# Kernel optimization log

Hardware: AMD Instinct MI355X
Metric: run time of the kernel (lower is better)

Reference implementation:

```python
import jax, jax.numpy as jnp
import numpy as np

THRESHOLD = 0.5
NEG_POS_RATIO = 3
ALPHA = 1.0
N_CLASSES = 81


def xy_to_cxcy(xy):
    return jnp.concatenate([(xy[..., :2] + xy[..., 2:]) / 2.0,
                            xy[..., 2:] - xy[..., :2]], axis=-1)


def cxcy_to_xy(cxcy):
    return jnp.concatenate([cxcy[..., :2] - cxcy[..., 2:] / 2.0,
                            cxcy[..., :2] + cxcy[..., 2:] / 2.0], axis=-1)


def cxcy_to_gcxgcy(cxcy, priors_cxcy):
    # SSD encoding with standard variances (0.1 for center, 0.2 for size)
    g_cxcy = (cxcy[..., :2] - priors_cxcy[..., :2]) / (priors_cxcy[..., 2:] / 10.0)
    g_wh = jnp.log(cxcy[..., 2:] / priors_cxcy[..., 2:]) * 5.0
    return jnp.concatenate([g_cxcy, g_wh], axis=-1)


def iou_pairwise(a_xy, b_xy):
    # a_xy: (N, O, 4), b_xy: (P, 4) -> (N, O, P)
    lt = jnp.maximum(a_xy[..., :, None, :2], b_xy[None, None, :, :2])
    rb = jnp.minimum(a_xy[..., :, None, 2:], b_xy[None, None, :, 2:])
    wh = jnp.clip(rb - lt, 0.0)
    inter = wh[..., 0] * wh[..., 1]
    area_a = (a_xy[..., 2] - a_xy[..., 0]) * (a_xy[..., 3] - a_xy[..., 1])
    area_b = (b_xy[:, 2] - b_xy[:, 0]) * (b_xy[:, 3] - b_xy[:, 1])
    union = area_a[..., :, None] + area_b[None, None, :] - inter
    return inter / union


def setup_inputs() -> dict:
    key = jax.random.key(0)
    k1, k2, k3, k4, k5, k6, k7 = jax.random.split(key, 7)
    N, P, C, O = 32, 8732, N_CLASSES, 16
    predicted_locs = jax.random.normal(k1, (N, P, 4), dtype=jnp.float32)
    predicted_scores = jax.random.normal(k2, (N, P, C), dtype=jnp.float32)
    # ground-truth boxes: build valid cxcy then convert to xy in [0, 1]
    b_cxy = jax.random.uniform(k3, (N, O, 2), minval=0.2, maxval=0.8)
    b_wh = jax.random.uniform(k4, (N, O, 2), minval=0.05, maxval=0.3)
    boxes = cxcy_to_xy(jnp.concatenate([b_cxy, b_wh], axis=-1)).astype(jnp.float32)
    labels = jax.random.randint(k5, (N, O), 1, C).astype(jnp.int32)  # 0 = background
    # priors in cxcy, valid (positive wh)
    p_cxy = jax.random.uniform(k6, (P, 2), minval=0.05, maxval=0.95)
    p_wh = jax.random.uniform(k7, (P, 2), minval=0.05, maxval=0.4)
    priors_cxcy = jnp.concatenate([p_cxy, p_wh], axis=-1).astype(jnp.float32)
    return {"predicted_locs": predicted_locs, "predicted_scores": predicted_scores,
            "boxes": boxes, "labels": labels, "priors_cxcy": priors_cxcy}


def reference(predicted_locs, predicted_scores, boxes, labels, priors_cxcy):
    N, P, C = predicted_scores.shape
    O = boxes.shape[1]
    priors_xy = cxcy_to_xy(priors_cxcy)  # (P, 4)

    overlap = iou_pairwise(boxes, priors_xy)            # (N, O, P)
    overlap_for_each_prior = overlap.max(axis=1)        # (N, P)
    object_for_each_prior = overlap.argmax(axis=1)      # (N, P)
    prior_for_each_object = overlap.argmax(axis=2)      # (N, O)

    obj_ids = jnp.arange(O)

    def assign(ofp, ovl, pfo):
        # force each object to be matched to its best prior with overlap 1
        ofp = ofp.at[pfo].set(obj_ids)
        ovl = ovl.at[pfo].set(1.0)
        return ofp, ovl

    object_for_each_prior, overlap_for_each_prior = jax.vmap(assign)(
        object_for_each_prior, overlap_for_each_prior, prior_for_each_object)

    label_for_each_prior = jnp.take_along_axis(labels, object_for_each_prior, axis=1)  # (N, P)
    true_classes = jnp.where(overlap_for_each_prior < THRESHOLD, 0, label_for_each_prior)

    matched_boxes = jnp.take_along_axis(
        boxes, object_for_each_prior[..., None], axis=1)  # (N, P, 4)
    true_locs = cxcy_to_gcxgcy(xy_to_cxcy(matched_boxes), priors_cxcy)

    positive = true_classes != 0                          # (N, P)
    pos_f = positive.astype(predicted_locs.dtype)

    # localization loss (L1, reduction='none' in original despite the name)
    loc_per_prior = jnp.abs(predicted_locs - true_locs).sum(axis=-1)  # (N, P)
    n_pos_total = pos_f.sum()
    loc_loss = (loc_per_prior * pos_f).sum() / (4.0 * n_pos_total)

    # confidence loss (cross entropy per prior)
    logp = jax.nn.log_softmax(predicted_scores, axis=-1)
    ce = -jnp.take_along_axis(logp, true_classes[..., None], axis=-1)[..., 0]  # (N, P)

    conf_loss_pos = (ce * pos_f).sum()
    ce_neg = jnp.where(positive, 0.0, ce)
    ce_neg_sorted = -jnp.sort(-ce_neg, axis=1)            # descending
    n_positives = positive.sum(axis=1)                    # (N,)
    hard = (jnp.arange(P)[None, :] < (NEG_POS_RATIO * n_positives)[:, None]).astype(ce.dtype)
    conf_loss_hard_neg = (ce_neg_sorted * hard).sum()
    conf_loss = (conf_loss_hard_neg + conf_loss_pos) / n_pos_total

    return conf_loss + ALPHA * loc_loss
```

## Files before the change

kernel.cpp:

```cpp
#include <hip/hip_runtime.h>
#include <hip/hip_bf16.h>
#include <stdint.h>

#define BLOCK 256
#define MAXO 64
#define TK_THREADS 1024
#define CK_MAX 4096

__global__ void match_object_kernel(const float* __restrict__ boxes,
                                    const float* __restrict__ priors,
                                    int* __restrict__ pfop,
                                    float* __restrict__ acc, int* __restrict__ n_pos,
                                    unsigned* __restrict__ done, int N, int P, int O) {
    __shared__ unsigned long long swm[4];
    int idx = blockIdx.x, tid = threadIdx.x;
    if (idx == 0) {
        for (int j = tid; j < N; j += BLOCK) n_pos[j] = 0;
        if (tid >= 64 && tid < 67) acc[tid - 64] = 0.f;
        if (tid == 96) *done = 0u;
    }
    const float* b = boxes + (size_t)idx * 4;
    float bx0 = b[0], by0 = b[1], bx1 = b[2], by1 = b[3];
    float areaa = (bx1 - bx0) * (by1 - by0);

    unsigned long long best = 0ULL;
    for (int p = tid; p < P; p += BLOCK) {
        float4 pr = ((const float4*)priors)[p];
        float px0 = pr.x - pr.z * 0.5f, py0 = pr.y - pr.w * 0.5f;
        float px1 = pr.x + pr.z * 0.5f, py1 = pr.y + pr.w * 0.5f;
        float areab = (px1 - px0) * (py1 - py0);
        float ltx = fmaxf(bx0, px0), lty = fmaxf(by0, py0);
        float rbx = fminf(bx1, px1), rby = fminf(by1, py1);
        float wx = fmaxf(rbx - ltx, 0.f), wy = fmaxf(rby - lty, 0.f);
        float inter = wx * wy;
        float iou = inter / (areaa + areab - inter);
        unsigned long long cand = (((unsigned long long)__float_as_uint(iou)) << 32) |
                                  (unsigned long long)(0xFFFFFFFFu - (unsigned)p);
        if (cand > best) best = cand;
    }
    #pragma unroll
    for (int off = 32; off >= 1; off >>= 1) {
        unsigned long long other = __shfl_down(best, off);
        if (other > best) best = other;
    }
    if ((tid & 63) == 0) swm[tid >> 6] = best;
    __syncthreads();
    if (tid == 0) {
        unsigned long long r = swm[0];
        for (int w = 1; w < BLOCK / 64; ++w) if (swm[w] > r) r = swm[w];
        pfop[idx] = (int)(0xFFFFFFFFu - (unsigned)(r & 0xFFFFFFFFull));
    }
}

__global__ void __launch_bounds__(256, 4)
fused_match_ce_kernel(const float* __restrict__ boxes,
                      const float* __restrict__ priors,
                      const float* __restrict__ locs,
                      const int* __restrict__ labels,
                      const int* __restrict__ pfop,
                      const float* __restrict__ scores,
                      float* __restrict__ ce_neg,
                      float* __restrict__ acc, int* __restrict__ n_pos,
                      int N, int P, int O) {
    __shared__ float sbx[MAXO * 4];
    __shared__ float sarea[MAXO];
    __shared__ int   spf[MAXO];
    __shared__ int   slab[MAXO];
    __shared__ float sredf[8];
    __shared__ int   sredi[4];
    int n = blockIdx.y, tid = threadIdx.x;
    if (tid < O * 4) sbx[tid] = boxes[(size_t)n * O * 4 + tid];
    if (tid >= 128 && tid < 128 + O) spf[tid - 128]  = pfop[n * O + (tid - 128)];
    if (tid >= 192 && tid < 192 + O) slab[tid - 192] = labels[n * O + (tid - 192)];
    __syncthreads();
    if (tid < O)
        sarea[tid] = (sbx[tid*4+2] - sbx[tid*4+0]) * (sbx[tid*4+3] - sbx[tid*4+1]);
    __syncthreads();

    int p = blockIdx.x * BLOCK + tid;
    bool valid = p < P;
    float my_loc = 0.f, my_pce = 0.f; int my_pos = 0;

    if (valid) {
        size_t t = (size_t)n * P + p;

        float4 pr = ((const float4*)priors)[p];

        int lane = tid & 63;
        int s = lane & 3;
        const float4* q = (const float4*)scores + (t >> 2) * 81;
        int g0q = (s == 0) ? 0 : (20 * s + 1);
        const float4* qa = q + g0q;

        float4 v[19];
        #pragma unroll
        for (int j = 0; j < 19; ++j) v[j] = qa[j];
        float4 v19 = q[19];
        float4 vb  = q[20 * (s + 1)];
        __builtin_amdgcn_sched_barrier(0);

        float px0 = pr.x - pr.z * 0.5f, py0 = pr.y - pr.w * 0.5f;
        float px1 = pr.x + pr.z * 0.5f, py1 = pr.y + pr.w * 0.5f;
        float areab = (px1 - px0) * (py1 - py0);

        float best = -1.f; int bo = 0;
        for (int o = 0; o < O; ++o) {
            float ltx = fmaxf(sbx[o*4+0], px0);
            float lty = fmaxf(sbx[o*4+1], py0);
            float rbx = fminf(sbx[o*4+2], px1);
            float rby = fminf(sbx[o*4+3], py1);
            float wx = fmaxf(rbx - ltx, 0.f), wy = fmaxf(rby - lty, 0.f);
            float inter = wx * wy;
            float iou = inter / (sarea[o] + areab - inter);
            if (iou > best) { best = iou; bo = o; }
        }
        int fo = -1;
        for (int o = 0; o < O; ++o) if (spf[o] == p) fo = o;
        int obj; float ov;
        if (fo >= 0) { obj = fo; ov = 1.0f; }
        else         { obj = bo; ov = best; }
        int tc = (ov < 0.5f) ? 0 : slab[obj];
        if (tc != 0) {
            my_pos = 1;
            float x0 = sbx[obj*4+0], y0 = sbx[obj*4+1], x1 = sbx[obj*4+2], y1 = sbx[obj*4+3];
            float cx = (x0 + x1) * 0.5f, cy = (y0 + y1) * 0.5f;
            float w = x1 - x0, h = y1 - y0;
            float g0 = (cx - pr.x) / (pr.z / 10.0f);
            float g1 = (cy - pr.y) / (pr.w / 10.0f);
            float g2 = logf(w / pr.z) * 5.0f;
            float g3 = logf(h / pr.w) * 5.0f;
            const float* pl = locs + t * 4;
            my_loc = fabsf(pl[0]-g0) + fabsf(pl[1]-g1) + fabsf(pl[2]-g2) + fabsf(pl[3]-g3);
        }

        float a0 = 0.f, a1 = 0.f, a2 = 0.f, a3 = 0.f;
        #pragma unroll
        for (int j = 0; j < 19; ++j) {
            a0 += __expf(v[j].x); a1 += __expf(v[j].y);
            a2 += __expf(v[j].z); a3 += __expf(v[j].w);
        }
        float A = (a0 + a1) + (a2 + a3);
        if (s == 0) A += __expf(v19.x) + __expf(v19.y) + __expf(v19.z) + __expf(v19.w);
        float B = 0.f;
        {
            float ex = __expf(vb.x), ey = __expf(vb.y), ez = __expf(vb.z), ew = __expf(vb.w);
            A += ex;
            A += (s >= 1) ? ey : 0.f;   B += (s >= 1) ? 0.f : ey;
            A += (s >= 2) ? ez : 0.f;   B += (s >= 2) ? 0.f : ez;
            A += (s == 3) ? ew : 0.f;   B += (s == 3) ? 0.f : ew;
        }
        int src = (lane & ~3) | ((s + 3) & 3);
        float l = A + __shfl(B, src);

        float stc = scores[t * 81 + tc];
        float ce = logf(l) - stc;
        ce_neg[t] = (tc != 0) ? 0.f : ce;
        if (tc != 0) my_pce = ce;
    }

    #pragma unroll
    for (int off = 32; off >= 1; off >>= 1) {
        my_loc += __shfl_down(my_loc, off);
        my_pce += __shfl_down(my_pce, off);
        my_pos += __shfl_down(my_pos, off);
    }
    if ((tid & 63) == 0) {
        int w = tid >> 6;
        sredf[w] = my_loc; sredf[4 + w] = my_pce; sredi[w] = my_pos;
    }
    __syncthreads();
    if (tid == 0) {
        float L  = (sredf[0] + sredf[1]) + (sredf[2] + sredf[3]);
        float Pp = (sredf[4] + sredf[5]) + (sredf[6] + sredf[7]);
        int  np  = sredi[0] + sredi[1] + sredi[2] + sredi[3];
        if (L  != 0.f) atomicAdd(&acc[0], L);
        if (Pp != 0.f) atomicAdd(&acc[1], Pp);
        if (np)        atomicAdd(&n_pos[n], np);
    }
}

__global__ void match_prior_kernel(const float* __restrict__ boxes,
                                   const float* __restrict__ priors,
                                   const float* __restrict__ locs,
                                   const int* __restrict__ labels,
                                   const int* __restrict__ pfop,
                                   int* __restrict__ tcarr,
                                   float* __restrict__ acc, int* __restrict__ n_pos,
                                   int N, int P, int O) {
    __shared__ float sbx[MAXO * 4];
    __shared__ float sarea[MAXO];
    __shared__ int   spf[MAXO];
    __shared__ int   slab[MAXO];
    int n = blockIdx.y, tid = threadIdx.x;
    if (tid < O * 4) sbx[tid] = boxes[(size_t)n * O * 4 + tid];
    if (tid >= 128 && tid < 128 + O) spf[tid - 128]  = pfop[n * O + (tid - 128)];
    if (tid >= 192 && tid < 192 + O) slab[tid - 192] = labels[n * O + (tid - 192)];
    __syncthreads();
    if (tid < O)
        sarea[tid] = (sbx[tid*4+2] - sbx[tid*4+0]) * (sbx[tid*4+3] - sbx[tid*4+1]);
    __syncthreads();

    int p = blockIdx.x * BLOCK + tid;
    bool valid = p < P;
    float my_loc = 0.f; int my_pos = 0;
    if (valid) {
        float4 pr = ((const float4*)priors)[p];
        float px0 = pr.x - pr.z * 0.5f, py0 = pr.y - pr.w * 0.5f;
        float px1 = pr.x + pr.z * 0.5f, py1 = pr.y + pr.w * 0.5f;
        float areab = (px1 - px0) * (py1 - py0);

        float best = -1.f; int bo = 0;
        for (int o = 0; o < O; ++o) {
            float ltx = fmaxf(sbx[o*4+0], px0);
            float lty = fmaxf(sbx[o*4+1], py0);
            float rbx = fminf(sbx[o*4+2], px1);
            float rby = fminf(sbx[o*4+3], py1);
            float wx = fmaxf(rbx - ltx, 0.f), wy = fmaxf(rby - lty, 0.f);
            float inter = wx * wy;
            float iou = inter / (sarea[o] + areab - inter);
            if (iou > best) { best = iou; bo = o; }
        }
        int fo = -1;
        for (int o = 0; o < O; ++o) if (spf[o] == p) fo = o;
        int obj; float ov;
        if (fo >= 0) { obj = fo; ov = 1.0f; }
        else         { obj = bo; ov = best; }
        int lab = slab[obj];
        int tc = (ov < 0.5f) ? 0 : lab;
        tcarr[(size_t)n * P + p] = tc;
        if (tc != 0) {
            my_pos = 1;
            float x0 = sbx[obj*4+0], y0 = sbx[obj*4+1], x1 = sbx[obj*4+2], y1 = sbx[obj*4+3];
            float cx = (x0 + x1) * 0.5f, cy = (y0 + y1) * 0.5f;
            float w = x1 - x0, h = y1 - y0;
            float g0 = (cx - pr.x) / (pr.z / 10.0f);
            float g1 = (cy - pr.y) / (pr.w / 10.0f);
            float g2 = logf(w / pr.z) * 5.0f;
            float g3 = logf(h / pr.w) * 5.0f;
            const float* pl = locs + ((size_t)n * P + p) * 4;
            my_loc = fabsf(pl[0]-g0) + fabsf(pl[1]-g1) + fabsf(pl[2]-g2) + fabsf(pl[3]-g3);
        }
    }
    #pragma unroll
    for (int off = 32; off >= 1; off >>= 1) {
        my_loc += __shfl_down(my_loc, off);
        my_pos += __shfl_down(my_pos, off);
    }
    if ((tid & 63) == 0 && my_pos) {
        atomicAdd(&acc[0], my_loc);
        atomicAdd(&n_pos[n], my_pos);
    }
}

__global__ void loss_generic_kernel(const float* __restrict__ scores,
                                    const int* __restrict__ tcarr,
                                    float* __restrict__ ce_neg, float* __restrict__ acc,
                                    int NP, int C) {
    int t = blockIdx.x * blockDim.x + threadIdx.x;
    if (t >= NP) return;
    int tc = tcarr[t];
    const float* s = scores + (size_t)t * C;
    float m = -3.0e38f;
    for (int j = 0; j < C; ++j) m = fmaxf(m, s[j]);
    float l = 0.f, stc = 0.f;
    for (int j = 0; j < C; ++j) {
        float v = s[j];
        l += __expf(v - m);
        if (j == tc) stc = v;
    }
    float ce = m + logf(l) - stc;
    bool pos = (tc != 0);
    ce_neg[t] = pos ? 0.f : ce;
    if (pos) atomicAdd(&acc[1], ce);
}

__global__ void topk_final_kernel(const float* __restrict__ ce_neg,
                                  const int* __restrict__ n_pos,
                                  float* __restrict__ acc, unsigned* __restrict__ done,
                                  int N, int P, unsigned* __restrict__ out) {
    __shared__ unsigned skeys[8732];
    __shared__ int hist[4096];
    __shared__ int part[1024];
    __shared__ int s_tb, s_ca, s_tb2, s_ca2, s_cnt;
    __shared__ float shf[16];
    int n = blockIdx.x, tid = threadIdx.x;
    int k = 3 * n_pos[n]; if (k > P) k = P;
    float bsum = 0.f;

    if (k > 0) {
        const float* row = ce_neg + (size_t)n * P;
        for (int i = tid; i < P; i += TK_THREADS) skeys[i] = __float_as_uint(row[i]);
        #pragma unroll
        for (int b = 0; b < 4; ++b) hist[tid * 4 + b] = 0;
        __syncthreads();

        for (int i = tid; i < P; i += TK_THREADS) atomicAdd(&hist[skeys[i] >> 20], 1);
        __syncthreads();
        int h0 = hist[tid*4], h1 = hist[tid*4+1], h2 = hist[tid*4+2], h3 = hist[tid*4+3];
        part[tid] = h0 + h1 + h2 + h3;
        __syncthreads();
        for (int s = 1; s < 1024; s <<= 1) {
            int v = part[tid] + ((tid + s < 1024) ? part[tid + s] : 0);
            __syncthreads();
            part[tid] = v;
            __syncthreads();
        }
        int sfx = (tid + 1 < 1024) ? part[tid + 1] : 0;
        int sf3 = sfx, sf2 = sfx + h3, sf1 = sf2 + h2, sf0 = sf1 + h1;
        if (sf0 < k && k <= sf0 + h0) { s_tb = tid*4;   s_ca = sf0; }
        if (sf1 < k && k <= sf1 + h1) { s_tb = tid*4+1; s_ca = sf1; }
        if (sf2 < k && k <= sf2 + h2) { s_tb = tid*4+2; s_ca = sf2; }
        if (sf3 < k && k <= sf3 + h3) { s_tb = tid*4+3; s_ca = sf3; }
        __syncthreads();
        int tb = s_tb, kk = k - s_ca;

        if (tid < 256) part[tid] = 0;
        __syncthreads();
        float ssum = 0.f;
        for (int i = tid; i < P; i += TK_THREADS) {
            unsigned key = skeys[i];
            int bin = key >> 20;
            if (bin > tb) ssum += __uint_as_float(key);
            else if (bin == tb) atomicAdd(&part[(key >> 12) & 255u], 1);
        }
        __syncthreads();
        if (tid < 256) {
            int cum = 0;
            for (int b = tid + 1; b < 256; ++b) cum += part[b];
            int h = part[tid];
            if (cum < kk && kk <= cum + h) { s_tb2 = tid; s_ca2 = cum; }
        }
        if (tid == 0) s_cnt = 0;
        __syncthreads();
        int tb2 = s_tb2, kk2 = kk - s_ca2;

        unsigned* ckeys = (unsigned*)hist;
        for (int i = tid; i < P; i += TK_THREADS) {
            unsigned key = skeys[i];
            if ((int)(key >> 20) == tb) {
                int b2 = (key >> 12) & 255u;
                if (b2 > tb2) ssum += __uint_as_float(key);
                else if (b2 == tb2) {
                    int slot = atomicAdd(&s_cnt, 1);
                    if (slot < CK_MAX) ckeys[slot] = key;
                }
            }
        }
        __syncthreads();
        int m = s_cnt; if (m > CK_MAX) m = CK_MAX;
        for (int i = tid; i < m; i += TK_THREADS) {
            unsigned key = ckeys[i];
            int rank = 0;
            for (int j = 0; j < m; ++j) {
                unsigned kj = ckeys[j];
                rank += (kj > key) || (kj == key && j < i);
            }
            if (rank < kk2) ssum += __uint_as_float(key);
        }
        #pragma unroll
        for (int off = 32; off >= 1; off >>= 1) ssum += __shfl_down(ssum, off);
        __syncthreads();
        if ((tid & 63) == 0) shf[tid >> 6] = ssum;
        __syncthreads();
        float tot = 0.f;
        for (int i = 0; i < 16; ++i) tot += shf[i];
        bsum = tot;
    }

    if (tid == 0) {
        if (bsum != 0.f) atomicAdd(&acc[2], bsum);
        __threadfence();
        unsigned old = atomicAdd(done, 1u);
        if (old == (unsigned)(N - 1)) {
            float a0 = atomicAdd(&acc[0], 0.f);
            float a1 = atomicAdd(&acc[1], 0.f);
            float a2 = atomicAdd(&acc[2], 0.f);
            int tot = 0;
            for (int i = 0; i < N; ++i) tot += n_pos[i];
            float npos = (float)tot;
            float conf = (a2 + a1) / npos;
            float loc  = a0 / (4.f * npos);
            float loss = conf + loc;
            unsigned ub = __float_as_uint(loss);
            unsigned r = (ub + 0x7FFFu + ((ub >> 16) & 1u)) >> 16;
            out[0] = (r << 16) | r;
        }
    }
}

extern "C" void kernel_launch(void* const* d_in, const int* in_sizes, int n_in,
                              void* d_out, int out_size, void* d_ws, size_t ws_size,
                              hipStream_t stream) {
    const float* locs   = (const float*)d_in[0];
    const float* scores = (const float*)d_in[1];
    const float* boxes  = (const float*)d_in[2];
    const int*   labels = (const int*)d_in[3];
    const float* priors = (const float*)d_in[4];

    int P = in_sizes[4] / 4;
    long long NPl = in_sizes[0] / 4;
    int N = (int)(NPl / P);
    int C = (int)((long long)in_sizes[1] / NPl);
    int O = in_sizes[3] / N;
    size_t NP = (size_t)N * P;

    char* ws = (char*)d_ws;
    float*    acc   = (float*)ws;     ws += 16;
    unsigned* done  = (unsigned*)ws;  ws += 16;
    int*      n_pos = (int*)ws;       ws += (size_t)N * 4;
    int*      pfop  = (int*)ws;       ws += (size_t)N * O * 4;
    int*      tcarr = (int*)ws;       ws += NP * 4;
    float*    ce_neg= (float*)ws;     ws += NP * 4;

    match_object_kernel<<<N * O, BLOCK, 0, stream>>>(boxes, priors, pfop, acc, n_pos,
                                                     done, N, P, O);
    int gx = (P + BLOCK - 1) / BLOCK;
    if (C == 81 && (P % 4) == 0 && O <= MAXO) {
        fused_match_ce_kernel<<<dim3(gx, N), BLOCK, 0, stream>>>(
            boxes, priors, locs, labels, pfop, scores, ce_neg, acc, n_pos, N, P, O);
    } else {
        match_prior_kernel<<<dim3(gx, N), BLOCK, 0, stream>>>(boxes, priors, locs, labels,
                                                              pfop, tcarr, acc, n_pos, N, P, O);
        loss_generic_kernel<<<(int)((NP + BLOCK - 1) / BLOCK), BLOCK, 0, stream>>>(
            scores, tcarr, ce_neg, acc, (int)NP, C);
    }
    topk_final_kernel<<<N, TK_THREADS, 0, stream>>>(ce_neg, n_pos, acc, done, N, P,
                                                    (unsigned*)d_out);
}
```

Before: 193.2 us.

## Stage score tiles into LDS via async global_load_lds overlapped with matching

The fused match/CE kernel now uses 128-thread blocks and copies each block's contiguous score tile straight into LDS with the global_load_lds builtin, issued before the IoU matching so the copy overlaps that compute. The logsumexp and the gather of the target-class score then read from LDS instead of holding 80+ floats per thread in registers, and priors and locs are loaded as float4 up front. This removes register pressure and allows fully coalesced wide loads, at the cost of about 40KB of LDS per block, which limits how many blocks fit per CU. The box areas are also recomputed inline rather than kept in shared memory.

```diff
diff --git a/kernel.cpp b/kernel.cpp
--- a/kernel.cpp
+++ b/kernel.cpp
@@ -3,9 +3,13 @@
 #include <stdint.h>
 
 #define BLOCK 256
+#define FBLOCK 128
 #define MAXO 64
 #define TK_THREADS 1024
 #define CK_MAX 4096
+
+typedef const unsigned int __attribute__((address_space(1))) guint_t;
+typedef unsigned int __attribute__((address_space(3))) luint_t;
 
 __global__ void match_object_kernel(const float* __restrict__ boxes,
                                     const float* __restrict__ priors,
@@ -52,7 +56,7 @@
     }
 }
 
-__global__ void __launch_bounds__(256, 4)
+__global__ void __launch_bounds__(FBLOCK)
 fused_match_ce_kernel(const float* __restrict__ boxes,
                       const float* __restrict__ priors,
                       const float* __restrict__ locs,
@@ -62,56 +66,57 @@
                       float* __restrict__ ce_neg,
                       float* __restrict__ acc, int* __restrict__ n_pos,
                       int N, int P, int O) {
+    __shared__ float4 sstage[FBLOCK * 81 / 4];
     __shared__ float sbx[MAXO * 4];
-    __shared__ float sarea[MAXO];
     __shared__ int   spf[MAXO];
     __shared__ int   slab[MAXO];
-    __shared__ float sredf[8];
-    __shared__ int   sredi[4];
+    __shared__ float sredf[4];
+    __shared__ int   sredi[2];
     int n = blockIdx.y, tid = threadIdx.x;
-    if (tid < O * 4) sbx[tid] = boxes[(size_t)n * O * 4 + tid];
-    if (tid >= 128 && tid < 128 + O) spf[tid - 128]  = pfop[n * O + (tid - 128)];
-    if (tid >= 192 && tid < 192 + O) slab[tid - 192] = labels[n * O + (tid - 192)];
-    __syncthreads();
-    if (tid < O)
-        sarea[tid] = (sbx[tid*4+2] - sbx[tid*4+0]) * (sbx[tid*4+3] - sbx[tid*4+1]);
-    __syncthreads();
-
-    int p = blockIdx.x * BLOCK + tid;
-    bool valid = p < P;
-    float my_loc = 0.f, my_pce = 0.f; int my_pos = 0;
-
+    int p0 = blockIdx.x * FBLOCK;
+    int rows = P - p0; if (rows > FBLOCK) rows = FBLOCK;
+    int p = p0 + tid;
+    bool valid = tid < rows;
+
+    for (int i = tid; i < O * 4; i += FBLOCK) sbx[i] = boxes[(size_t)n * O * 4 + i];
+    for (int i = tid; i < O; i += FBLOCK) { spf[i] = pfop[n * O + i]; slab[i] = labels[n * O + i]; }
+    float4 pr = make_float4(0.f, 0.f, 0.f, 0.f);
+    float4 pl = make_float4(0.f, 0.f, 0.f, 0.f);
     if (valid) {
-        size_t t = (size_t)n * P + p;
-
-        float4 pr = ((const float4*)priors)[p];
-
-        int lane = tid & 63;
-        int s = lane & 3;
-        const float4* q = (const float4*)scores + (t >> 2) * 81;
-        int g0q = (s == 0) ? 0 : (20 * s + 1);
-        const float4* qa = q + g0q;
-
-        float4 v[19];
-        #pragma unroll
-        for (int j = 0; j < 19; ++j) v[j] = qa[j];
-        float4 v19 = q[19];
-        float4 vb  = q[20 * (s + 1)];
-        __builtin_amdgcn_sched_barrier(0);
-
+        pr = ((const float4*)priors)[p];
+        pl = ((const float4*)locs)[(size_t)n * P + p];
+    }
+    __syncthreads();
+
+    const float* gbase = scores + ((size_t)n * P + p0) * 81;
+    int valid_f4 = rows * 81 / 4;
+    int wbase = tid & ~63;
+    #pragma unroll
+    for (int j = 0; j < 21; ++j) {
+        int idx = j * FBLOCK + tid;
+        if (idx < valid_f4) {
+            __builtin_amdgcn_global_load_lds(
+                (guint_t*)(gbase + (size_t)idx * 4),
+                (luint_t*)&sstage[j * FBLOCK + wbase],
+                16, 0, 0);
+        }
+    }
+
+    float my_loc = 0.f, my_pce = 0.f; int my_pos = 0; int tc = 0;
+    if (valid) {
         float px0 = pr.x - pr.z * 0.5f, py0 = pr.y - pr.w * 0.5f;
         float px1 = pr.x + pr.z * 0.5f, py1 = pr.y + pr.w * 0.5f;
         float areab = (px1 - px0) * (py1 - py0);
 
         float best = -1.f; int bo = 0;
         for (int o = 0; o < O; ++o) {
-            float ltx = fmaxf(sbx[o*4+0], px0);
-            float lty = fmaxf(sbx[o*4+1], py0);
-            float rbx = fminf(sbx[o*4+2], px1);
-            float rby = fminf(sbx[o*4+3], py1);
+            float x0 = sbx[o*4+0], y0 = sbx[o*4+1], x1 = sbx[o*4+2], y1 = sbx[o*4+3];
+            float ltx = fmaxf(x0, px0), lty = fmaxf(y0, py0);
+            float rbx = fminf(x1, px1), rby = fminf(y1, py1);
             float wx = fmaxf(rbx - ltx, 0.f), wy = fmaxf(rby - lty, 0.f);
             float inter = wx * wy;
-            float iou = inter / (sarea[o] + areab - inter);
+            float areao = (x1 - x0) * (y1 - y0);
+            float iou = inter / (areao + areab - inter);
             if (iou > best) { best = iou; bo = o; }
         }
         int fo = -1;
@@ -119,7 +124,7 @@
         int obj; float ov;
         if (fo >= 0) { obj = fo; ov = 1.0f; }
         else         { obj = bo; ov = best; }
-        int tc = (ov < 0.5f) ? 0 : slab[obj];
+        tc = (ov < 0.5f) ? 0 : slab[obj];
         if (tc != 0) {
             my_pos = 1;
             float x0 = sbx[obj*4+0], y0 = sbx[obj*4+1], x1 = sbx[obj*4+2], y1 = sbx[obj*4+3];
@@ -129,15 +134,27 @@
             float g1 = (cy - pr.y) / (pr.w / 10.0f);
             float g2 = logf(w / pr.z) * 5.0f;
             float g3 = logf(h / pr.w) * 5.0f;
-            const float* pl = locs + t * 4;
-            my_loc = fabsf(pl[0]-g0) + fabsf(pl[1]-g1) + fabsf(pl[2]-g2) + fabsf(pl[3]-g3);
-        }
+            my_loc = fabsf(pl.x-g0) + fabsf(pl.y-g1) + fabsf(pl.z-g2) + fabsf(pl.w-g3);
+        }
+    }
+
+    __syncthreads();
+
+    if (valid) {
+        int lane = tid & 63;
+        int s = tid & 3;
+        const float4* q = &sstage[(tid >> 2) * 81];
+        int g0q = (s == 0) ? 0 : (20 * s + 1);
+        const float4* qa = q + g0q;
 
         float a0 = 0.f, a1 = 0.f, a2 = 0.f, a3 = 0.f;
+        float4 v19 = q[19];
+        float4 vb  = q[20 * (s + 1)];
         #pragma unroll
         for (int j = 0; j < 19; ++j) {
-            a0 += __expf(v[j].x); a1 += __expf(v[j].y);
-            a2 += __expf(v[j].z); a3 += __expf(v[j].w);
+            float4 v = qa[j];
+            a0 += __expf(v.x); a1 += __expf(v.y);
+            a2 += __expf(v.z); a3 += __expf(v.w);
         }
         float A = (a0 + a1) + (a2 + a3);
         if (s == 0) A += __expf(v19.x) + __expf(v19.y) + __expf(v19.z) + __expf(v19.w);
@@ -152,9 +169,9 @@
         int src = (lane & ~3) | ((s + 3) & 3);
         float l = A + __shfl(B, src);
 
-        float stc = scores[t * 81 + tc];
+        float stc = ((const float*)sstage)[tid * 81 + tc];
         float ce = logf(l) - stc;
-        ce_neg[t] = (tc != 0) ? 0.f : ce;
+        ce_neg[(size_t)n * P + p] = (tc != 0) ? 0.f : ce;
         if (tc != 0) my_pce = ce;
     }
 
@@ -166,13 +183,13 @@
     }
     if ((tid & 63) == 0) {
         int w = tid >> 6;
-        sredf[w] = my_loc; sredf[4 + w] = my_pce; sredi[w] = my_pos;
+        sredf[w] = my_loc; sredf[2 + w] = my_pce; sredi[w] = my_pos;
     }
     __syncthreads();
     if (tid == 0) {
-        float L  = (sredf[0] + sredf[1]) + (sredf[2] + sredf[3]);
-        float Pp = (sredf[4] + sredf[5]) + (sredf[6] + sredf[7]);
-        int  np  = sredi[0] + sredi[1] + sredi[2] + sredi[3];
+        float L  = sredf[0] + sredf[1];
+        float Pp = sredf[2] + sredf[3];
+        int  np  = sredi[0] + sredi[1];
         if (L  != 0.f) atomicAdd(&acc[0], L);
         if (Pp != 0.f) atomicAdd(&acc[1], Pp);
         if (np)        atomicAdd(&n_pos[n], np);
@@ -414,11 +431,12 @@
 
     match_object_kernel<<<N * O, BLOCK, 0, stream>>>(boxes, priors, pfop, acc, n_pos,
                                                      done, N, P, O);
-    int gx = (P + BLOCK - 1) / BLOCK;
     if (C == 81 && (P % 4) == 0 && O <= MAXO) {
-        fused_match_ce_kernel<<<dim3(gx, N), BLOCK, 0, stream>>>(
+        int gx = (P + FBLOCK - 1) / FBLOCK;
+        fused_match_ce_kernel<<<dim3(gx, N), FBLOCK, 0, stream>>>(
             boxes, priors, locs, labels, pfop, scores, ce_neg, acc, n_pos, N, P, O);
     } else {
+        int gx = (P + BLOCK - 1) / BLOCK;
         match_prior_kernel<<<dim3(gx, N), BLOCK, 0, stream>>>(boxes, priors, locs, labels,
                                                               pfop, tcarr, acc, n_pos, N, P, O);
         loss_generic_kernel<<<(int)((NP + BLOCK - 1) / BLOCK), BLOCK, 0, stream>>>(
```

After: 222.3 us. +15.1%, slower.

## Issue score loads via inline asm before the barrier and overlap them with matching

Applied to the files above, without the earlier changes.

The 21 dwordx4 score loads are now issued through inline global_load asm before the IoU matching loop, with a single explicit s_waitcnt placed before the exp-sum. Matching math then runs while the loads are in flight, and out-of-range threads use a clamped address. Priors and locs are loaded as float4 before the first syncthreads, and the per-object box area is recomputed inline, which removes one barrier and the sarea shared array. The block-level shared-memory reduction is replaced by per-wave atomics, which trades fewer barriers for more atomic traffic.

```diff
diff --git a/kernel.cpp b/kernel.cpp
--- a/kernel.cpp
+++ b/kernel.cpp
@@ -6,6 +6,12 @@
 #define MAXO 64
 #define TK_THREADS 1024
 #define CK_MAX 4096
+
+typedef float f32x4 __attribute__((ext_vector_type(4)));
+
+#define GLD(dst, base, off) \
+    asm volatile("global_load_dwordx4 %0, %1, off offset:" #off \
+                 : "=v"(dst) : "v"(base))
 
 __global__ void match_object_kernel(const float* __restrict__ boxes,
                                     const float* __restrict__ priors,
@@ -52,7 +58,7 @@
     }
 }
 
-__global__ void __launch_bounds__(256, 4)
+__global__ void __launch_bounds__(BLOCK, 4)
 fused_match_ce_kernel(const float* __restrict__ boxes,
                       const float* __restrict__ priors,
                       const float* __restrict__ locs,
@@ -63,55 +69,58 @@
                       float* __restrict__ acc, int* __restrict__ n_pos,
                       int N, int P, int O) {
     __shared__ float sbx[MAXO * 4];
-    __shared__ float sarea[MAXO];
     __shared__ int   spf[MAXO];
     __shared__ int   slab[MAXO];
-    __shared__ float sredf[8];
-    __shared__ int   sredi[4];
     int n = blockIdx.y, tid = threadIdx.x;
+    int p = blockIdx.x * BLOCK + tid;
+    bool valid = p < P;
+    int lane = tid & 63;
+    int s = tid & 3;
+
     if (tid < O * 4) sbx[tid] = boxes[(size_t)n * O * 4 + tid];
     if (tid >= 128 && tid < 128 + O) spf[tid - 128]  = pfop[n * O + (tid - 128)];
     if (tid >= 192 && tid < 192 + O) slab[tid - 192] = labels[n * O + (tid - 192)];
+    float4 pr = make_float4(0.f, 0.f, 1.f, 1.f);
+    float4 pl = make_float4(0.f, 0.f, 0.f, 0.f);
+    size_t t = (size_t)n * P + p;
+    if (valid) {
+        pr = ((const float4*)priors)[p];
+        pl = ((const float4*)locs)[t];
+    }
     __syncthreads();
-    if (tid < O)
-        sarea[tid] = (sbx[tid*4+2] - sbx[tid*4+0]) * (sbx[tid*4+3] - sbx[tid*4+1]);
-    __syncthreads();
-
-    int p = blockIdx.x * BLOCK + tid;
-    bool valid = p < P;
-    float my_loc = 0.f, my_pce = 0.f; int my_pos = 0;
-
+
+    size_t NPt = (size_t)N * P;
+    size_t tcl = (t < NPt) ? t : (NPt - 4);
+    const f32x4* q  = (const f32x4*)scores + (tcl >> 2) * 81;
+    const f32x4* qa = q + ((s == 0) ? 0 : (20 * s + 1));
+    const f32x4* vbp = q + 20 * (s + 1);
+
+    f32x4 v[19]; f32x4 v19, vb;
+    GLD(v[0],  qa, 0);   GLD(v[1],  qa, 16);  GLD(v[2],  qa, 32);
+    GLD(v[3],  qa, 48);  GLD(v[4],  qa, 64);  GLD(v[5],  qa, 80);
+    GLD(v[6],  qa, 96);  GLD(v[7],  qa, 112); GLD(v[8],  qa, 128);
+    GLD(v[9],  qa, 144); GLD(v[10], qa, 160); GLD(v[11], qa, 176);
+    GLD(v[12], qa, 192); GLD(v[13], qa, 208); GLD(v[14], qa, 224);
+    GLD(v[15], qa, 240); GLD(v[16], qa, 256); GLD(v[17], qa, 272);
+    GLD(v[18], qa, 288);
+    GLD(v19, q, 304);
+    GLD(vb,  vbp, 0);
+
+    float my_loc = 0.f, my_pce = 0.f; int my_pos = 0; int tc = 0;
     if (valid) {
-        size_t t = (size_t)n * P + p;
-
-        float4 pr = ((const float4*)priors)[p];
-
-        int lane = tid & 63;
-        int s = lane & 3;
-        const float4* q = (const float4*)scores + (t >> 2) * 81;
-        int g0q = (s == 0) ? 0 : (20 * s + 1);
-        const float4* qa = q + g0q;
-
-        float4 v[19];
-        #pragma unroll
-        for (int j = 0; j < 19; ++j) v[j] = qa[j];
-        float4 v19 = q[19];
-        float4 vb  = q[20 * (s + 1)];
-        __builtin_amdgcn_sched_barrier(0);
-
         float px0 = pr.x - pr.z * 0.5f, py0 = pr.y - pr.w * 0.5f;
         float px1 = pr.x + pr.z * 0.5f, py1 = pr.y + pr.w * 0.5f;
         float areab = (px1 - px0) * (py1 - py0);
 
         float best = -1.f; int bo = 0;
         for (int o = 0; o < O; ++o) {
-            float ltx = fmaxf(sbx[o*4+0], px0);
-            float lty = fmaxf(sbx[o*4+1], py0);
-            float rbx = fminf(sbx[o*4+2], px1);
-            float rby = fminf(sbx[o*4+3], py1);
+            float x0 = sbx[o*4+0], y0 = sbx[o*4+1], x1 = sbx[o*4+2], y1 = sbx[o*4+3];
+            float ltx = fmaxf(x0, px0), lty = fmaxf(y0, py0);
+            float rbx = fminf(x1, px1), rby = fminf(y1, py1);
             float wx = fmaxf(rbx - ltx, 0.f), wy = fmaxf(rby - lty, 0.f);
             float inter = wx * wy;
-            float iou = inter / (sarea[o] + areab - inter);
+            float areao = (x1 - x0) * (y1 - y0);
+            float iou = inter / (areao + areab - inter);
             if (iou > best) { best = iou; bo = o; }
         }
         int fo = -1;
@@ -119,7 +128,7 @@
         int obj; float ov;
         if (fo >= 0) { obj = fo; ov = 1.0f; }
         else         { obj = bo; ov = best; }
-        int tc = (ov < 0.5f) ? 0 : slab[obj];
+        tc = (ov < 0.5f) ? 0 : slab[obj];
         if (tc != 0) {
             my_pos = 1;
             float x0 = sbx[obj*4+0], y0 = sbx[obj*4+1], x1 = sbx[obj*4+2], y1 = sbx[obj*4+3];
@@ -129,21 +138,25 @@
             float g1 = (cy - pr.y) / (pr.w / 10.0f);
             float g2 = logf(w / pr.z) * 5.0f;
             float g3 = logf(h / pr.w) * 5.0f;
-            const float* pl = locs + t * 4;
-            my_loc = fabsf(pl[0]-g0) + fabsf(pl[1]-g1) + fabsf(pl[2]-g2) + fabsf(pl[3]-g3);
-        }
-
+            my_loc = fabsf(pl.x-g0) + fabsf(pl.y-g1) + fabsf(pl.z-g2) + fabsf(pl.w-g3);
+        }
+    }
+
+    asm volatile("s_waitcnt vmcnt(0)" ::: "memory");
+    __builtin_amdgcn_sched_barrier(0);
+
+    if (valid) {
         float a0 = 0.f, a1 = 0.f, a2 = 0.f, a3 = 0.f;
         #pragma unroll
         for (int j = 0; j < 19; ++j) {
-            a0 += __expf(v[j].x); a1 += __expf(v[j].y);
-            a2 += __expf(v[j].z); a3 += __expf(v[j].w);
+            a0 += __expf(v[j][0]); a1 += __expf(v[j][1]);
+            a2 += __expf(v[j][2]); a3 += __expf(v[j][3]);
         }
         float A = (a0 + a1) + (a2 + a3);
-        if (s == 0) A += __expf(v19.x) + __expf(v19.y) + __expf(v19.z) + __expf(v19.w);
+        if (s == 0) A += __expf(v19[0]) + __expf(v19[1]) + __expf(v19[2]) + __expf(v19[3]);
         float B = 0.f;
         {
-            float ex = __expf(vb.x), ey = __expf(vb.y), ez = __expf(vb.z), ew = __expf(vb.w);
+            float ex = __expf(vb[0]), ey = __expf(vb[1]), ez = __expf(vb[2]), ew = __expf(vb[3]);
             A += ex;
             A += (s >= 1) ? ey : 0.f;   B += (s >= 1) ? 0.f : ey;
             A += (s >= 2) ? ez : 0.f;   B += (s >= 2) ? 0.f : ez;
@@ -165,17 +178,11 @@
         my_pos += __shfl_down(my_pos, off);
     }
     if ((tid & 63) == 0) {
-        int w = tid >> 6;
-        sredf[w] = my_loc; sredf[4 + w] = my_pce; sredi[w] = my_pos;
-    }
-    __syncthreads();
-    if (tid == 0) {
-        float L  = (sredf[0] + sredf[1]) + (sredf[2] + sredf[3]);
-        float Pp = (sredf[4] + sredf[5]) + (sredf[6] + sredf[7]);
-        int  np  = sredi[0] + sredi[1] + sredi[2] + sredi[3];
-        if (L  != 0.f) atomicAdd(&acc[0], L);
-        if (Pp != 0.f) atomicAdd(&acc[1], Pp);
-        if (np)        atomicAdd(&n_pos[n], np);
+        if (my_pos) {
+            atomicAdd(&acc[0], my_loc);
+            atomicAdd(&n_pos[n], my_pos);
+        }
+        if (my_pce != 0.f) atomicAdd(&acc[1], my_pce);
     }
 }
 
```

Measured after the change: 273.4 us. 41.5% more time.
